# Optimization experiments

Hardware: AMD Instinct MI355X
Metric: run time of the kernel (lower is better)

The kernel has to match this reference:

```python
import jax, jax.numpy as jnp
import numpy as np

N, E, F, H, HEADS, L, G = 16384, 262144, 16, 128, 4, 5, 128
DFF = 4 * H
EPS = 1e-5

def _bn(h, g, b):
    m = h.mean(axis=0)
    v = h.var(axis=0)
    return g * (h - m) / jnp.sqrt(v + EPS) + b

def setup_inputs():
    key = jax.random.key(0)
    ks = jax.random.split(key, 20)
    rn = lambda k, s, fan: jax.random.normal(k, s, jnp.float32) / np.float32(np.sqrt(fan))
    return {
        'x': jax.random.normal(ks[0], (N, F), jnp.float32),
        'edge_index': jax.random.randint(ks[1], (2, E), 0, N),
        'batch_index': jnp.sort(jax.random.randint(ks[2], (N,), 0, G)),
        'embW': rn(ks[3], (F, H), F), 'embb': jnp.zeros((H,), jnp.float32),
        'emb_g': jnp.ones((H,), jnp.float32), 'emb_be': jnp.zeros((H,), jnp.float32),
        'Wq': rn(ks[4], (L, H, HEADS * H), H), 'bq': jnp.zeros((L, HEADS * H), jnp.float32),
        'Wk': rn(ks[5], (L, H, HEADS * H), H), 'bk': jnp.zeros((L, HEADS * H), jnp.float32),
        'Wv': rn(ks[6], (L, H, HEADS * H), H), 'bv': jnp.zeros((L, HEADS * H), jnp.float32),
        'Wskip': rn(ks[7], (L, H, H), H), 'bskip': jnp.zeros((L, H), jnp.float32),
        'Wbeta': rn(ks[8], (L, 3 * H, 1), 3 * H),
        'W1': rn(ks[9], (L, H, DFF), H), 'b1': jnp.zeros((L, DFF), jnp.float32),
        'g1': jnp.ones((L, DFF), jnp.float32), 'be1': jnp.zeros((L, DFF), jnp.float32),
        'W2': rn(ks[10], (L, DFF, H), DFF), 'b2': jnp.zeros((L, H), jnp.float32),
        'predW': rn(ks[11], (H, 1), H), 'predb': jnp.zeros((1,), jnp.float32),
    }

def reference(x, edge_index, batch_index, embW, embb, emb_g, emb_be, Wq, bq, Wk, bk, Wv, bv, Wskip, bskip, Wbeta, W1, b1, g1, be1, W2, b2, predW, predb):
    src, dst = edge_index[0], edge_index[1]
    h = jax.nn.gelu(_bn(x @ embW + embb, emb_g, emb_be), approximate=False)
    scale = jnp.float32(1.0 / np.sqrt(H))  # sqrt(out_channels) per PyG TransformerConv

    def layer(h, p):
        Wq_, bq_, Wk_, bk_, Wv_, bv_, Ws_, bs_, Wb_, W1_, b1_, g1_, be1_, W2_, b2_ = p
        q = (h @ Wq_ + bq_).reshape(N, HEADS, H)
        k = (h @ Wk_ + bk_).reshape(N, HEADS, H)
        v = (h @ Wv_ + bv_).reshape(N, HEADS, H)
        logits = jnp.einsum('ehc,ehc->eh', q[dst], k[src]) * scale  # [E, HEADS]
        m = jax.ops.segment_max(logits, dst, num_segments=N)
        p_e = jnp.exp(logits - m[dst])
        denom = jax.ops.segment_sum(p_e, dst, num_segments=N) + 1e-16
        agg = jax.ops.segment_sum(p_e[:, :, None] * v[src], dst, num_segments=N)
        out = (agg / denom[:, :, None]).mean(axis=1)  # concat=False -> mean over heads
        x_r = h @ Ws_ + bs_
        beta = jax.nn.sigmoid(jnp.concatenate([out, x_r, out - x_r], axis=-1) @ Wb_)  # [N,1]
        out = beta * x_r + (1.0 - beta) * out
        hh = jax.nn.gelu(_bn(out @ W1_ + b1_, g1_, be1_), approximate=False)
        return hh @ W2_ + b2_

    def step(carry, p):
        return layer(carry, p), None

    h, _ = jax.lax.scan(step, h, (Wq, bq, Wk, bk, Wv, bv, Wskip, bskip, Wbeta, W1, b1, g1, be1, W2, b2))
    pooled = jax.ops.segment_max(h, batch_index, num_segments=G)  # MaxAggregation
    return (pooled @ predW + predb).reshape(-1)
```

## Files before the change

### kernel.cpp

```cpp
#include <hip/hip_runtime.h>
#include <hip/hip_bf16.h>

using bf16 = __hip_bfloat16;
typedef __attribute__((ext_vector_type(8))) short bf16x8;
typedef __attribute__((ext_vector_type(4))) float f32x4;

constexpr int N_   = 16384;
constexpr int E_   = 262144;
constexpr int F_   = 16;
constexpr int H_   = 128;
constexpr int NF1_ = 640;
constexpr int DFF_ = 512;
constexpr int G_   = 128;
constexpr int L_   = 5;
constexpr float EPS_ = 1e-5f;

constexpr int WCAT1SZ = NF1_ * 128;
constexpr int W1TSZ   = 512 * 128;
constexpr int W2TSZ   = 512 * 128;
constexpr int WVSSZ   = 128 * 512;
constexpr int TRBLKS  = 5 * 144;

__device__ __forceinline__ float gelu_f(float x) {
  return 0.5f * x * (1.0f + erff(x * 0.70710678118654752440f));
}

__device__ __forceinline__ void unpack8(const uint4 w, float* f) {
  f[0] = __uint_as_float(w.x << 16); f[1] = __uint_as_float(w.x & 0xFFFF0000u);
  f[2] = __uint_as_float(w.y << 16); f[3] = __uint_as_float(w.y & 0xFFFF0000u);
  f[4] = __uint_as_float(w.z << 16); f[5] = __uint_as_float(w.z & 0xFFFF0000u);
  f[6] = __uint_as_float(w.w << 16); f[7] = __uint_as_float(w.w & 0xFFFF0000u);
}

__global__ __launch_bounds__(256) void k_ptrans(
    const float* __restrict__ Ws, const float* __restrict__ W1,
    const float* __restrict__ W2, const float* __restrict__ bs,
    const float* __restrict__ bv,
    bf16* __restrict__ Wcat1, bf16* __restrict__ W1t, bf16* __restrict__ W2t,
    float* __restrict__ bcat, float* __restrict__ bvm) {
  __shared__ float lds[32][33];
  const int b = blockIdx.x;
  if (b >= TRBLKS) {
    int j = (b - TRBLKS) * 256 + threadIdx.x;
    if (j < 5 * NF1_) {
      int l = j / NF1_, c = j % NF1_;
      if (c >= 512) bcat[j] = bs[l * 128 + (c - 512)];
    } else if (j < 5 * NF1_ + 5 * 128) {
      int j2 = j - 5 * NF1_;
      int l = j2 / 128, n = j2 % 128;
      bvm[j2] = 0.25f * (bv[l * 512 + n] + bv[l * 512 + 128 + n]
                       + bv[l * 512 + 256 + n] + bv[l * 512 + 384 + n]);
    }
    return;
  }
  const int l = b / 144, t = b % 144;
  const float* src; int C; bf16* dst; int dld; int nof; int tt;
  if (t < 16) {
    tt = t;
    src = Ws + (size_t)l * 128 * 128; C = 128;
    dst = Wcat1 + (size_t)l * WCAT1SZ; dld = 128; nof = 512;
  } else if (t < 80) {
    tt = t - 16;
    src = W1 + (size_t)l * 128 * 512; C = 512;
    dst = W1t + (size_t)l * W1TSZ; dld = 128; nof = 0;
  } else {
    tt = t - 80;
    src = W2 + (size_t)l * 512 * 128; C = 128;
    dst = W2t + (size_t)l * W2TSZ; dld = 512; nof = 0;
  }
  const int tpr = C >> 5;
  const int r0 = (tt / tpr) * 32, c0 = (tt % tpr) * 32;
  const int j = threadIdx.x & 31, g = threadIdx.x >> 5;
#pragma unroll
  for (int ii = 0; ii < 4; ++ii) {
    int i = g * 4 + ii;
    lds[i][j] = src[(size_t)(r0 + i) * C + c0 + j];
  }
  __syncthreads();
#pragma unroll
  for (int ii = 0; ii < 4; ++ii) {
    int i = g * 4 + ii;
    dst[(size_t)(nof + c0 + i) * dld + r0 + j] = __float2bfloat16(lds[j][i]);
  }
}

__global__ __launch_bounds__(256) void k_wvprep(const float* __restrict__ Wv,
                                                bf16* __restrict__ Wvs) {
  __shared__ float lds[32][33];
  const int b = blockIdx.x;
  const int l = b / 64, rest = b % 64;
  const int h = rest / 16, tt = rest % 16;
  const int r0 = (tt / 4) * 32, c0 = (tt % 4) * 32;
  const float* src = Wv + (size_t)l * 128 * 512 + h * 128;
  bf16* dst = Wvs + (size_t)l * WVSSZ;
  const int j = threadIdx.x & 31, g = threadIdx.x >> 5;
#pragma unroll
  for (int ii = 0; ii < 4; ++ii) {
    int i = g * 4 + ii;
    lds[i][j] = src[(size_t)(r0 + i) * 512 + c0 + j];
  }
  __syncthreads();
#pragma unroll
  for (int ii = 0; ii < 4; ++ii) {
    int i = g * 4 + ii;
    dst[(size_t)(c0 + i) * 512 + h * 128 + r0 + j] = __float2bfloat16(0.25f * lds[j][i]);
  }
}

__global__ __launch_bounds__(256) void k_gmat(
    const float* __restrict__ Wq, const float* __restrict__ Wk,
    const float* __restrict__ bq,
    bf16* __restrict__ Wcat1, float* __restrict__ bcat) {
  __shared__ float lq[32][132];
  __shared__ float lk[32][132];
  const int l = blockIdx.x >> 2, h = blockIdx.x & 3;
  const int half = blockIdx.y;
  const int tid = threadIdx.x;
  const int c = tid & 127, ch = tid >> 7;
  const int cp0 = half * 64 + ch * 32;
  const float* wqL = Wq + (size_t)l * 128 * 512 + h * 128;
  const float* wkL = Wk + (size_t)l * 128 * 512 + h * 128;
  float acc[32];
#pragma unroll
  for (int j = 0; j < 32; ++j) acc[j] = 0.f;
  for (int a0 = 0; a0 < 128; a0 += 32) {
    __syncthreads();
#pragma unroll
    for (int q4 = 0; q4 < 4; ++q4) {
      int f4 = tid * 4 + q4;
      int row = f4 >> 3, af = f4 & 7;
      float4 gq = *reinterpret_cast<const float4*>(wqL + (size_t)row * 512 + a0 + af * 4);
      float4 gk = *reinterpret_cast<const float4*>(wkL + (size_t)row * 512 + a0 + af * 4);
      lq[af * 4 + 0][row] = gq.x; lq[af * 4 + 1][row] = gq.y;
      lq[af * 4 + 2][row] = gq.z; lq[af * 4 + 3][row] = gq.w;
      lk[af * 4 + 0][row] = gk.x; lk[af * 4 + 1][row] = gk.y;
      lk[af * 4 + 2][row] = gk.z; lk[af * 4 + 3][row] = gk.w;
    }
    __syncthreads();
    for (int a = 0; a < 32; ++a) {
      float wq = lq[a][c];
#pragma unroll
      for (int j = 0; j < 32; ++j) acc[j] = fmaf(wq, lk[a][cp0 + j], acc[j]);
    }
  }
  bf16* gt = Wcat1 + (size_t)l * WCAT1SZ;
#pragma unroll
  for (int j = 0; j < 32; ++j)
    gt[(size_t)(h * 128 + cp0 + j) * 128 + c] = __float2bfloat16(acc[j]);
  if (half == 0 && ch == 0) {
    float s = 0.f;
    const float* wkr = wkL + (size_t)c * 512;
    const float* bqh = bq + (size_t)l * 512 + h * 128;
    for (int a = 0; a < 128; ++a) s = fmaf(wkr[a], bqh[a], s);
    bcat[(size_t)l * NF1_ + h * 128 + c] = s;
  }
}

__global__ __launch_bounds__(256) void k_embed2(const float* __restrict__ x,
    const float* __restrict__ W, const float* __restrict__ b,
    float* __restrict__ out, float* __restrict__ ss, float* __restrict__ sq) {
  __shared__ float xs[128][16];
  __shared__ float wsm[16][128];
  __shared__ float sr[2][128], qr[2][128];
  const int blk = blockIdx.x;
  const int t = threadIdx.x;
  for (int i = t; i < 16 * 128; i += 256) wsm[i >> 7][i & 127] = W[i];
  for (int i = t; i < 128 * 16; i += 256) xs[i >> 4][i & 15] = x[(size_t)blk * 2048 + i];
  __syncthreads();
  const int c = t & 127, rg = t >> 7;
  float bc = b[c];
  float s = 0.f, q = 0.f;
  for (int r = rg * 64; r < rg * 64 + 64; ++r) {
    float v = bc;
#pragma unroll
    for (int f = 0; f < 16; ++f) v = fmaf(xs[r][f], wsm[f][c], v);
    out[(size_t)(blk * 128 + r) * 128 + c] = v;
    s += v; q += v * v;
  }
  sr[rg][c] = s; qr[rg][c] = q;
  __syncthreads();
  if (t < 128) { ss[blk * 128 + t] = sr[0][t] + sr[1][t]; sq[blk * 128 + t] = qr[0][t] + qr[1][t]; }
}

template<int NC, int NP>
__global__ void k_bn_finalize(const float* __restrict__ sums, const float* __restrict__ sumsq,
                              const float* __restrict__ g, const float* __restrict__ be,
                              float* __restrict__ a, float* __restrict__ cc) {
  int c = blockIdx.x * 128 + threadIdx.x;
  if (c >= NC) return;
  float s = 0.f, q = 0.f;
  for (int b = 0; b < NP; ++b) { s += sums[(size_t)b * NC + c]; q += sumsq[(size_t)b * NC + c]; }
  float mean = s * (1.0f / N_);
  float var  = q * (1.0f / N_) - mean * mean;
  float inv  = rsqrtf(var + EPS_);
  float aa   = g[c] * inv;
  a[c]  = aa;
  cc[c] = be[c] - aa * mean;
}

template<int NC>
__global__ void k_bn_apply_gelu_cast(const float* __restrict__ xin, const float* __restrict__ a,
                                     const float* __restrict__ cc, bf16* __restrict__ outb) {
  int i4 = (blockIdx.x * 256 + threadIdx.x) * 4;
  int c = i4 & (NC - 1);
  float4 v = *reinterpret_cast<const float4*>(xin + i4);
  union { uint2 u2; bf16 h[4]; } pk;
  pk.h[0] = __float2bfloat16(gelu_f(fmaf(a[c + 0], v.x, cc[c + 0])));
  pk.h[1] = __float2bfloat16(gelu_f(fmaf(a[c + 1], v.y, cc[c + 1])));
  pk.h[2] = __float2bfloat16(gelu_f(fmaf(a[c + 2], v.z, cc[c + 2])));
  pk.h[3] = __float2bfloat16(gelu_f(fmaf(a[c + 3], v.w, cc[c + 3])));
  *reinterpret_cast<uint2*>(outb + i4) = pk.u2;
}

__global__ void k_count(const int* __restrict__ dst, int* __restrict__ deg) {
  int e = blockIdx.x * 256 + threadIdx.x;
  if (e < E_) atomicAdd(&deg[dst[e]], 1);
}

__global__ void k_bsum(const int* __restrict__ deg, int* __restrict__ bsum) {
  __shared__ int sh[256];
  int t = threadIdx.x;
  sh[t] = deg[blockIdx.x * 256 + t];
  __syncthreads();
  for (int d = 128; d > 0; d >>= 1) { if (t < d) sh[t] += sh[t + d]; __syncthreads(); }
  if (t == 0) bsum[blockIdx.x] = sh[0];
}

__global__ void k_boffs(const int* __restrict__ deg, const int* __restrict__ bsum,
                        int* __restrict__ offs) {
  __shared__ int sh[256];
  __shared__ int baseSh;
  int t = threadIdx.x;
  if (t < 64) {
    int v = bsum[t];
    int s = v;
    for (int d = 1; d < 64; d <<= 1) { int o = __shfl_up(s, d); if (t >= d) s += o; }
    if (t == (int)blockIdx.x) baseSh = s - v;
  }
  int v = deg[blockIdx.x * 256 + t];
  sh[t] = v;
  __syncthreads();
  for (int d = 1; d < 256; d <<= 1) {
    int add = (t >= d) ? sh[t - d] : 0;
    __syncthreads();
    sh[t] += add;
    __syncthreads();
  }
  offs[blockIdx.x * 256 + t] = baseSh + sh[t] - v;
  if (blockIdx.x == 63 && t == 255) offs[N_] = E_;
}

__global__ void k_scatter(const int* __restrict__ src, const int* __restrict__ dst,
                          const int* __restrict__ off, int* __restrict__ cursor,
                          int* __restrict__ srcs) {
  int e = blockIdx.x * 256 + threadIdx.x;
  if (e < E_) {
    int d = dst[e];
    int pos = off[d] + atomicAdd(&cursor[d], 1);
    srcs[pos] = src[e];
  }
}

template<int KDIM, int NOUT, int TM, int MODE>
__global__ __launch_bounds__(256) void k_mfma(
    const bf16* __restrict__ A, const bf16* __restrict__ BT,
    const float* __restrict__ bias,
    float* __restrict__ outF,
    float* __restrict__ zfp, float* __restrict__ xrp,
    float* __restrict__ ss, float* __restrict__ sq) {
  constexpr int MF = TM / 32;
  __shared__ bf16 As[TM][72];
  __shared__ bf16 Bs[128][72];
  __shared__ float sred[2][128], qred[2][128];
  const int tid = threadIdx.x;
  const int wid = tid >> 6, lane = tid & 63;
  const int wr = wid >> 1, wc = wid & 1;
  const int m0 = blockIdx.x * TM, n0 = blockIdx.y * 128;
  const int ln = lane & 15, lq = lane >> 4;
  f32x4 acc[MF][4];
#pragma unroll
  for (int i = 0; i < MF; ++i)
#pragma unroll
    for (int j = 0; j < 4; ++j) acc[i][j] = (f32x4){0.f, 0.f, 0.f, 0.f};

  for (int k0 = 0; k0 < KDIM; k0 += 64) {
#pragma unroll
    for (int u = tid; u < TM * 8; u += 256) {
      int r = u >> 3, c = u & 7;
      *(uint4*)(&As[r][c * 8]) = *(const uint4*)(A + (size_t)(m0 + r) * KDIM + k0 + c * 8);
    }
#pragma unroll
    for (int u = tid; u < 1024; u += 256) {
      int r = u >> 3, c = u & 7;
      *(uint4*)(&Bs[r][c * 8]) = *(const uint4*)(BT + (size_t)(n0 + r) * KDIM + k0 + c * 8);
    }
    __syncthreads();
#pragma unroll
    for (int kk = 0; kk < 2; ++kk) {
      bf16x8 af[MF], bg[4];
#pragma unroll
      for (int i = 0; i < MF; ++i)
        af[i] = *(const bf16x8*)(&As[wr * (TM / 2) + i * 16 + ln][kk * 32 + lq * 8]);
#pragma unroll
      for (int j = 0; j < 4; ++j)
        bg[j] = *(const bf16x8*)(&Bs[wc * 64 + j * 16 + ln][kk * 32 + lq * 8]);
#pragma unroll
      for (int i = 0; i < MF; ++i)
#pragma unroll
        for (int j = 0; j < 4; ++j)
          acc[i][j] = __builtin_amdgcn_mfma_f32_16x16x32_bf16(af[i], bg[j], acc[i][j], 0, 0, 0);
    }
    __syncthreads();
  }
  float ssj[4] = {0.f, 0.f, 0.f, 0.f}, sqj[4] = {0.f, 0.f, 0.f, 0.f};
#pragma unroll
  for (int i = 0; i < MF; ++i) {
#pragma unroll
    for (int j = 0; j < 4; ++j) {
      int gcol = n0 + wc * 64 + j * 16 + ln;
      float bv = bias[gcol];
      int row0 = m0 + wr * (TM / 2) + i * 16 + lq * 4;
#pragma unroll
      for (int qq = 0; qq < 4; ++qq) {
        float val = acc[i][j][qq] + bv;
        int row = row0 + qq;
        if (MODE == 3) {
          outF[(size_t)row * NOUT + gcol] = val;
          ssj[j] += val; sqj[j] += val * val;
        } else {
          if (gcol < 512) zfp[(size_t)row * 512 + gcol] = val;
          else            xrp[(size_t)row * H_ + (gcol - 512)] = val;
        }
      }
    }
  }
  if constexpr (MODE == 3) {
#pragma unroll
    for (int j = 0; j < 4; ++j) {
      ssj[j] += __shfl_xor(ssj[j], 16); ssj[j] += __shfl_xor(ssj[j], 32);
      sqj[j] += __shfl_xor(sqj[j], 16); sqj[j] += __shfl_xor(sqj[j], 32);
    }
    if (lq == 0) {
#pragma unroll
      for (int j = 0; j < 4; ++j) {
        sred[wr][wc * 64 + j * 16 + ln] = ssj[j];
        qred[wr][wc * 64 + j * 16 + ln] = sqj[j];
      }
    }
    __syncthreads();
    if (tid < 128) {
      ss[(size_t)blockIdx.x * NOUT + n0 + tid] = sred[0][tid] + sred[1][tid];
      sq[(size_t)blockIdx.x * NOUT + n0 + tid] = qred[0][tid] + qred[1][tid];
    }
  }
}

template<int KDIM, int NOUT, int CSPL, int MODE>
__global__ __launch_bounds__(256) void k_sgemm(
    const bf16* __restrict__ A, const bf16* __restrict__ BT,
    const float* __restrict__ bias,
    float* __restrict__ outF, bf16* __restrict__ outB) {
  constexpr int KS = KDIM / 32;
  constexpr int NCOL = NOUT / CSPL;
  constexpr int NFR = NCOL / 16;
  __shared__ bf16 Bs[NFR][KS][64][8];
  const int tid = threadIdx.x;
  const int wid = tid >> 6, lane = tid & 63;
  const int ln = lane & 15, lq = lane >> 4;
  const int nc0 = blockIdx.y * NCOL;
  for (int idx = tid; idx < NCOL * (KDIM / 8); idx += 256) {
    int col = idx / (KDIM / 8);
    int oct = idx % (KDIM / 8);
    uint4 w = *(const uint4*)(BT + (size_t)(nc0 + col) * KDIM + oct * 8);
    int ks = oct >> 2, q = oct & 3;
    *(uint4*)(&Bs[col >> 4][ks][q * 16 + (col & 15)][0]) = w;
  }
  __syncthreads();
  const int m0 = blockIdx.x * 64 + wid * 16;
  bf16x8 a[KS];
  const bf16* ap = A + (size_t)(m0 + ln) * KDIM + lq * 8;
#pragma unroll
  for (int ks = 0; ks < KS; ++ks) a[ks] = *(const bf16x8*)(ap + ks * 32);
  const int orow = m0 + lq * 4;
#pragma unroll
  for (int nf = 0; nf < NFR; ++nf) {
    f32x4 acc0 = (f32x4){0.f, 0.f, 0.f, 0.f};
    f32x4 acc1 = (f32x4){0.f, 0.f, 0.f, 0.f};
#pragma unroll
    for (int ks = 0; ks < KS; ks += 2) {
      acc0 = __builtin_amdgcn_mfma_f32_16x16x32_bf16(a[ks],     *(const bf16x8*)(&Bs[nf][ks][lane][0]),     acc0, 0, 0, 0);
      acc1 = __builtin_amdgcn_mfma_f32_16x16x32_bf16(a[ks + 1], *(const bf16x8*)(&Bs[nf][ks + 1][lane][0]), acc1, 0, 0, 0);
    }
    const int col = nc0 + nf * 16 + ln;
    float bv = 0.f;
    if constexpr (MODE == 6) bv = bias[col];
    float v0 = (acc0[0] + acc1[0]) + bv;
    float v1 = (acc0[1] + acc1[1]) + bv;
    float v2 = (acc0[2] + acc1[2]) + bv;
    float v3 = (acc0[3] + acc1[3]) + bv;
    outF[(size_t)(orow + 0) * NOUT + col] = v0;
    outF[(size_t)(orow + 1) * NOUT + col] = v1;
    outF[(size_t)(orow + 2) * NOUT + col] = v2;
    outF[(size_t)(orow + 3) * NOUT + col] = v3;
    if constexpr (MODE == 6) {
      outB[(size_t)(orow + 0) * NOUT + col] = __float2bfloat16(v0);
      outB[(size_t)(orow + 1) * NOUT + col] = __float2bfloat16(v1);
      outB[(size_t)(orow + 2) * NOUT + col] = __float2bfloat16(v2);
      outB[(size_t)(orow + 3) * NOUT + col] = __float2bfloat16(v3);
    }
  }
}

__global__ __launch_bounds__(256) void k_attn(const float* __restrict__ zf,
    const bf16* __restrict__ hb, const int* __restrict__ srcs,
    const int* __restrict__ off, bf16* __restrict__ aggB) {
  const int wave = threadIdx.x >> 6;
  const int lane = threadIdx.x & 63;
  const int bid = blockIdx.x;
  const int swz = ((bid & 7) << 9) | (bid >> 3);
  const int node = swz * 4 + wave;
  const int sub = lane & 15;
  const float scale = 0.08838834764831845f;
  float qf[8];
  {
    const float4* qp = reinterpret_cast<const float4*>(zf + (size_t)node * 512) + lane * 2;
    float4 a = qp[0], b = qp[1];
    qf[0]=a.x; qf[1]=a.y; qf[2]=a.z; qf[3]=a.w;
    qf[4]=b.x; qf[5]=b.y; qf[6]=b.z; qf[7]=b.w;
  }
  float m = -1e30f, den = 0.f;
  float acc[8] = {0.f, 0.f, 0.f, 0.f, 0.f, 0.f, 0.f, 0.f};
  const int s0 = off[node], s1 = off[node + 1];
  if (s0 < s1) {
    int i0 = srcs[s0];
    int i1 = (s0 + 1 < s1) ? srcs[s0 + 1] : i0;
    uint4 h0 = *(const uint4*)(hb + (size_t)i0 * 128 + sub * 8);
    uint4 h1 = *(const uint4*)(hb + (size_t)i1 * 128 + sub * 8);
    for (int t = s0; t < s1; t += 2) {
      int j0 = (t + 2 < s1) ? srcs[t + 2] : i0;
      int j1 = (t + 3 < s1) ? srcs[t + 3] : i0;
      uint4 nh0 = *(const uint4*)(hb + (size_t)j0 * 128 + sub * 8);
      uint4 nh1 = *(const uint4*)(hb + (size_t)j1 * 128 + sub * 8);
      {
        float hf[8]; unpack8(h0, hf);
        float p = hf[0]*qf[0]+hf[1]*qf[1]+hf[2]*qf[2]+hf[3]*qf[3]
                + hf[4]*qf[4]+hf[5]*qf[5]+hf[6]*qf[6]+hf[7]*qf[7];
        p += __shfl_xor(p, 1); p += __shfl_xor(p, 2);
        p += __shfl_xor(p, 4); p += __shfl_xor(p, 8);
        float logit = p * scale;
        if (logit > m + 8.f) {
          float co = __expf(m - logit);
          den *= co;
#pragma unroll
          for (int j = 0; j < 8; ++j) acc[j] *= co;
          m = logit;
        }
        float pe = __expf(logit - m);
        den += pe;
#pragma unroll
        for (int j = 0; j < 8; ++j) acc[j] = fmaf(pe, hf[j], acc[j]);
      }
      if (t + 1 < s1) {
        float hf[8]; unpack8(h1, hf);
        float p = hf[0]*qf[0]+hf[1]*qf[1]+hf[2]*qf[2]+hf[3]*qf[3]
                + hf[4]*qf[4]+hf[5]*qf[5]+hf[6]*qf[6]+hf[7]*qf[7];
        p += __shfl_xor(p, 1); p += __shfl_xor(p, 2);
        p += __shfl_xor(p, 4); p += __shfl_xor(p, 8);
        float logit = p * scale;
        if (logit > m + 8.f) {
          float co = __expf(m - logit);
          den *= co;
#pragma unroll
          for (int j = 0; j < 8; ++j) acc[j] *= co;
          m = logit;
        }
        float pe = __expf(logit - m);
        den += pe;
#pragma unroll
        for (int j = 0; j < 8; ++j) acc[j] = fmaf(pe, hf[j], acc[j]);
      }
      h0 = nh0; h1 = nh1;
    }
  }
  float inv = 1.f / (den + 1e-16f);
  union { uint4 u4; bf16 h[8]; } pk;
#pragma unroll
  for (int j = 0; j < 8; ++j) pk.h[j] = __float2bfloat16(acc[j] * inv);
  *reinterpret_cast<uint4*>(aggB + (size_t)node * 512 + lane * 8) = pk.u4;
}

__global__ __launch_bounds__(256) void k_beta(const float* __restrict__ out0,
    const float* __restrict__ xr, const float* __restrict__ Wb,
    const float* __restrict__ bvm, const int* __restrict__ off,
    bf16* __restrict__ gated) {
  const int wave = threadIdx.x >> 6;
  const int lane = threadIdx.x & 63;
  const int node = blockIdx.x * 4 + wave;
  const int c0 = lane * 2;
  bool hasE = off[node + 1] > off[node];
  const size_t base = (size_t)node * H_ + c0;
  float2 o = *reinterpret_cast<const float2*>(out0 + base);
  if (hasE) { o.x += bvm[c0]; o.y += bvm[c0 + 1]; }
  float2 xv = *reinterpret_cast<const float2*>(xr + base);
  float s = o.x * (Wb[c0] + Wb[256 + c0]) + xv.x * (Wb[128 + c0] - Wb[256 + c0])
          + o.y * (Wb[c0 + 1] + Wb[256 + c0 + 1]) + xv.y * (Wb[128 + c0 + 1] - Wb[256 + c0 + 1]);
#pragma unroll
  for (int d = 1; d < 64; d <<= 1) s += __shfl_xor(s, d);
  float beta = 1.f / (1.f + __expf(-s));
  union { unsigned u; bf16 h[2]; } pk;
  pk.h[0] = __float2bfloat16(beta * xv.x + (1.f - beta) * o.x);
  pk.h[1] = __float2bfloat16(beta * xv.y + (1.f - beta) * o.y);
  *reinterpret_cast<unsigned*>(gated + base) = pk.u;
}

__global__ __launch_bounds__(256) void k_poolpred(const float* __restrict__ h,
    const int* __restrict__ batch, const float* __restrict__ predW,
    const float* __restrict__ predb, float* __restrict__ out) {
  __shared__ float cm[2][128];
  __shared__ int range[2];
  const int g = blockIdx.x, t = threadIdx.x;
  if (t < 2) {
    int target = g + t;
    int lo = 0, hi = N_;
    while (lo < hi) { int mid = (lo + hi) >> 1; if (batch[mid] < target) lo = mid + 1; else hi = mid; }
    range[t] = lo;
  }
  __syncthreads();
  const int lo = range[0], hi = range[1];
  const int c = t & 127, rg = t >> 7;
  float m = -3.402823466e+38f;
  for (int r = lo + rg; r < hi; r += 2) m = fmaxf(m, h[(size_t)r * H_ + c]);
  cm[rg][c] = m;
  __syncthreads();
  if (t < 64) {
    float m0 = fmaxf(cm[0][t], cm[1][t]);
    float m1 = fmaxf(cm[0][t + 64], cm[1][t + 64]);
    float s = m0 * predW[t] + m1 * predW[t + 64];
#pragma unroll
    for (int d = 1; d < 64; d <<= 1) s += __shfl_xor(s, d);
    if (t == 0) out[g] = s + predb[0];
  }
}

extern "C" void kernel_launch(void* const* d_in, const int* in_sizes, int n_in,
                              void* d_out, int out_size, void* d_ws, size_t ws_size,
                              hipStream_t stream) {
  const float* x      = (const float*)d_in[0];
  const int*   edge   = (const int*)d_in[1];
  const int*   esrc   = edge;
  const int*   edst   = edge + E_;
  const int*   batch  = (const int*)d_in[2];
  const float* embW   = (const float*)d_in[3];
  const float* embb   = (const float*)d_in[4];
  const float* emb_g  = (const float*)d_in[5];
  const float* emb_be = (const float*)d_in[6];
  const float* Wq     = (const float*)d_in[7];
  const float* bq     = (const float*)d_in[8];
  const float* Wk     = (const float*)d_in[9];
  const float* Wv     = (const float*)d_in[11];
  const float* bv     = (const float*)d_in[12];
  const float* Wskip  = (const float*)d_in[13];
  const float* bskip  = (const float*)d_in[14];
  const float* Wbeta  = (const float*)d_in[15];
  const float* W1     = (const float*)d_in[16];
  const float* b1     = (const float*)d_in[17];
  const float* g1     = (const float*)d_in[18];
  const float* be1    = (const float*)d_in[19];
  const float* W2     = (const float*)d_in[20];
  const float* b2     = (const float*)d_in[21];
  const float* predW  = (const float*)d_in[22];
  const float* predb  = (const float*)d_in[23];

  float* ws = (float*)d_ws;
  size_t o = 0;
  auto alloc_f = [&](size_t n) { float* p = ws + o; o += n; return p; };
  float* A32   = alloc_f((size_t)N_ * 512);
  float* B32   = alloc_f((size_t)N_ * H_);
  float* xr    = alloc_f((size_t)N_ * H_);
  float* stats = alloc_f((size_t)2 * 128 * DFF_);
  float* a_c   = alloc_f(DFF_);
  float* c_c   = alloc_f(DFF_);
  float* bcat  = alloc_f(5 * NF1_);
  float* bvm   = alloc_f(5 * 128);
  bf16* bp = (bf16*)(ws + o);
  size_t ob = 0;
  auto alloc_b = [&](size_t n) { bf16* p = bp + ob; ob += n; return p; };
  bf16* aggB = alloc_b((size_t)N_ * 512);
  bf16* hb   = alloc_b((size_t)N_ * H_);
  bf16* gated= alloc_b((size_t)N_ * H_);
  bf16* Wcat1= alloc_b((size_t)5 * WCAT1SZ);
  bf16* W1t  = alloc_b((size_t)5 * W1TSZ);
  bf16* W2t  = alloc_b((size_t)5 * W2TSZ);
  bf16* Wvs  = alloc_b((size_t)5 * WVSSZ);
  int* deg    = (int*)(bp + ob);
  int* offs   = deg + N_;
  int* cursor = offs + N_ + 1;
  int* srcs   = cursor + N_;
  int* bsum   = srcs + E_;

  float* zf   = A32;  float* t1 = A32;
  float* out0 = B32;  float* h32 = B32;
  bf16*  t1b  = aggB;

  k_ptrans<<<TRBLKS + 15, 256, 0, stream>>>(Wskip, W1, W2, bskip, bv,
                                            Wcat1, W1t, W2t, bcat, bvm);
  k_wvprep<<<320, 256, 0, stream>>>(Wv, Wvs);
  k_gmat<<<dim3(20, 2), 256, 0, stream>>>(Wq, Wk, bq, Wcat1, bcat);

  hipMemsetAsync(deg, 0, N_ * sizeof(int), stream);
  hipMemsetAsync(cursor, 0, N_ * sizeof(int), stream);
  k_count  <<<E_ / 256, 256, 0, stream>>>(edst, deg);
  k_bsum   <<<64, 256, 0, stream>>>(deg, bsum);
  k_boffs  <<<64, 256, 0, stream>>>(deg, bsum, offs);
  k_scatter<<<E_ / 256, 256, 0, stream>>>(esrc, edst, offs, cursor, srcs);

  k_embed2<<<128, 256, 0, stream>>>(x, embW, embb, A32, stats, stats + 128 * 128);
  k_bn_finalize<128, 128><<<1, 128, 0, stream>>>(stats, stats + 128 * 128, emb_g, emb_be, a_c, c_c);
  k_bn_apply_gelu_cast<128><<<N_ * H_ / 1024, 256, 0, stream>>>(A32, a_c, c_c, hb);

  for (int l = 0; l < L_; ++l) {
    const float* Wb_ = Wbeta + (size_t)l * 3 * H_;
    const float* b1_ = b1 + (size_t)l * DFF_;
    const float* g1_ = g1 + (size_t)l * DFF_;
    const float* be1_= be1 + (size_t)l * DFF_;
    const float* b2_ = b2 + (size_t)l * H_;

    k_mfma<128, NF1_, 128, 2><<<dim3(N_ / 128, NF1_ / 128), 256, 0, stream>>>(
        hb, Wcat1 + (size_t)l * WCAT1SZ, bcat + (size_t)l * NF1_,
        nullptr, zf, xr, nullptr, nullptr);

    k_attn<<<N_ / 4, 256, 0, stream>>>(zf, hb, srcs, offs, aggB);

    k_sgemm<512, 128, 2, 5><<<dim3(N_ / 64, 2), 256, 0, stream>>>(
        aggB, Wvs + (size_t)l * WVSSZ, nullptr, out0, nullptr);

    k_beta<<<N_ / 4, 256, 0, stream>>>(out0, xr, Wb_, bvm + (size_t)l * 128, offs, gated);

    k_mfma<128, 512, 128, 3><<<dim3(N_ / 128, 4), 256, 0, stream>>>(
        gated, W1t + (size_t)l * W1TSZ, b1_,
        t1, nullptr, nullptr, stats, stats + 128 * 512);

    k_bn_finalize<512, 128><<<4, 128, 0, stream>>>(
        stats, stats + 128 * 512, g1_, be1_, a_c, c_c);

    k_bn_apply_gelu_cast<512><<<N_ * DFF_ / 1024, 256, 0, stream>>>(t1, a_c, c_c, t1b);

    k_sgemm<512, 128, 2, 6><<<dim3(N_ / 64, 2), 256, 0, stream>>>(
        t1b, W2t + (size_t)l * W2TSZ, b2_, h32, hb);
  }

  k_poolpred<<<G_, 256, 0, stream>>>(h32, batch, predW, predb, (float*)d_out);
}
```

Measured before the change: 685.5 us.

## Fuse BN-apply+GELU into W2 GEMM and move QKV GEMM to register-A sgemm

The separate BN-apply/GELU/bf16-cast pass over the 16384x512 FFN hidden tensor is removed. The W2 GEMM now reads fp32 t1 directly and applies the per-column affine, erf GELU and bf16 cast while loading its A fragments. The first per-layer projection GEMM (hb x Wcat1 into zf/xr) moves from the tiled LDS k_mfma kernel to the k_sgemm kernel, which keeps A in registers with a 5-way column split. The fused W2 path reads fp32 instead of bf16 and computes GELU redundantly in each of the two column-split blocks, trading one kernel and its round trip for extra reads and erf work.

```diff
diff --git a/kernel.cpp b/kernel.cpp
--- a/kernel.cpp
+++ b/kernel.cpp
@@ -266,7 +266,6 @@
     const bf16* __restrict__ A, const bf16* __restrict__ BT,
     const float* __restrict__ bias,
     float* __restrict__ outF,
-    float* __restrict__ zfp, float* __restrict__ xrp,
     float* __restrict__ ss, float* __restrict__ sq) {
   constexpr int MF = TM / 32;
   __shared__ bf16 As[TM][72];
@@ -324,46 +323,42 @@
       for (int qq = 0; qq < 4; ++qq) {
         float val = acc[i][j][qq] + bv;
         int row = row0 + qq;
-        if (MODE == 3) {
-          outF[(size_t)row * NOUT + gcol] = val;
-          ssj[j] += val; sqj[j] += val * val;
-        } else {
-          if (gcol < 512) zfp[(size_t)row * 512 + gcol] = val;
-          else            xrp[(size_t)row * H_ + (gcol - 512)] = val;
-        }
+        outF[(size_t)row * NOUT + gcol] = val;
+        ssj[j] += val; sqj[j] += val * val;
       }
     }
   }
-  if constexpr (MODE == 3) {
+#pragma unroll
+  for (int j = 0; j < 4; ++j) {
+    ssj[j] += __shfl_xor(ssj[j], 16); ssj[j] += __shfl_xor(ssj[j], 32);
+    sqj[j] += __shfl_xor(sqj[j], 16); sqj[j] += __shfl_xor(sqj[j], 32);
+  }
+  if (lq == 0) {
 #pragma unroll
     for (int j = 0; j < 4; ++j) {
-      ssj[j] += __shfl_xor(ssj[j], 16); ssj[j] += __shfl_xor(ssj[j], 32);
-      sqj[j] += __shfl_xor(sqj[j], 16); sqj[j] += __shfl_xor(sqj[j], 32);
-    }
-    if (lq == 0) {
-#pragma unroll
-      for (int j = 0; j < 4; ++j) {
-        sred[wr][wc * 64 + j * 16 + ln] = ssj[j];
-        qred[wr][wc * 64 + j * 16 + ln] = sqj[j];
-      }
-    }
-    __syncthreads();
-    if (tid < 128) {
-      ss[(size_t)blockIdx.x * NOUT + n0 + tid] = sred[0][tid] + sred[1][tid];
-      sq[(size_t)blockIdx.x * NOUT + n0 + tid] = qred[0][tid] + qred[1][tid];
-    }
+      sred[wr][wc * 64 + j * 16 + ln] = ssj[j];
+      qred[wr][wc * 64 + j * 16 + ln] = sqj[j];
+    }
+  }
+  __syncthreads();
+  if (tid < 128) {
+    ss[(size_t)blockIdx.x * NOUT + n0 + tid] = sred[0][tid] + sred[1][tid];
+    sq[(size_t)blockIdx.x * NOUT + n0 + tid] = qred[0][tid] + qred[1][tid];
   }
 }
 
 template<int KDIM, int NOUT, int CSPL, int MODE>
 __global__ __launch_bounds__(256) void k_sgemm(
-    const bf16* __restrict__ A, const bf16* __restrict__ BT,
-    const float* __restrict__ bias,
-    float* __restrict__ outF, bf16* __restrict__ outB) {
+    const bf16* __restrict__ A, const float* __restrict__ Af,
+    const bf16* __restrict__ BT, const float* __restrict__ bias,
+    float* __restrict__ outF, bf16* __restrict__ outB,
+    float* __restrict__ zfp, float* __restrict__ xrp,
+    const float* __restrict__ aCol, const float* __restrict__ cCol) {
   constexpr int KS = KDIM / 32;
   constexpr int NCOL = NOUT / CSPL;
   constexpr int NFR = NCOL / 16;
   __shared__ bf16 Bs[NFR][KS][64][8];
+  __shared__ float aS[MODE == 7 ? KDIM : 1], cS[MODE == 7 ? KDIM : 1];
   const int tid = threadIdx.x;
   const int wid = tid >> 6, lane = tid & 63;
   const int ln = lane & 15, lq = lane >> 4;
@@ -375,12 +370,31 @@
     int ks = oct >> 2, q = oct & 3;
     *(uint4*)(&Bs[col >> 4][ks][q * 16 + (col & 15)][0]) = w;
   }
+  if constexpr (MODE == 7) {
+    for (int i = tid; i < KDIM; i += 256) { aS[i] = aCol[i]; cS[i] = cCol[i]; }
+  }
   __syncthreads();
   const int m0 = blockIdx.x * 64 + wid * 16;
   bf16x8 a[KS];
-  const bf16* ap = A + (size_t)(m0 + ln) * KDIM + lq * 8;
-#pragma unroll
-  for (int ks = 0; ks < KS; ++ks) a[ks] = *(const bf16x8*)(ap + ks * 32);
+  if constexpr (MODE == 7) {
+    const float* ap = Af + (size_t)(m0 + ln) * KDIM + lq * 8;
+#pragma unroll
+    for (int ks = 0; ks < KS; ++ks) {
+      float4 f0 = *(const float4*)(ap + ks * 32);
+      float4 f1 = *(const float4*)(ap + ks * 32 + 4);
+      float f[8] = {f0.x, f0.y, f0.z, f0.w, f1.x, f1.y, f1.z, f1.w};
+      int colb = lq * 8 + ks * 32;
+      union { bf16x8 v; bf16 h[8]; } pk;
+#pragma unroll
+      for (int j = 0; j < 8; ++j)
+        pk.h[j] = __float2bfloat16(gelu_f(fmaf(aS[colb + j], f[j], cS[colb + j])));
+      a[ks] = pk.v;
+    }
+  } else {
+    const bf16* ap = A + (size_t)(m0 + ln) * KDIM + lq * 8;
+#pragma unroll
+    for (int ks = 0; ks < KS; ++ks) a[ks] = *(const bf16x8*)(ap + ks * 32);
+  }
   const int orow = m0 + lq * 4;
 #pragma unroll
   for (int nf = 0; nf < NFR; ++nf) {
@@ -393,20 +407,35 @@
     }
     const int col = nc0 + nf * 16 + ln;
     float bv = 0.f;
-    if constexpr (MODE == 6) bv = bias[col];
+    if constexpr (MODE != 5) bv = bias[col];
     float v0 = (acc0[0] + acc1[0]) + bv;
     float v1 = (acc0[1] + acc1[1]) + bv;
     float v2 = (acc0[2] + acc1[2]) + bv;
     float v3 = (acc0[3] + acc1[3]) + bv;
-    outF[(size_t)(orow + 0) * NOUT + col] = v0;
-    outF[(size_t)(orow + 1) * NOUT + col] = v1;
-    outF[(size_t)(orow + 2) * NOUT + col] = v2;
-    outF[(size_t)(orow + 3) * NOUT + col] = v3;
-    if constexpr (MODE == 6) {
-      outB[(size_t)(orow + 0) * NOUT + col] = __float2bfloat16(v0);
-      outB[(size_t)(orow + 1) * NOUT + col] = __float2bfloat16(v1);
-      outB[(size_t)(orow + 2) * NOUT + col] = __float2bfloat16(v2);
-      outB[(size_t)(orow + 3) * NOUT + col] = __float2bfloat16(v3);
+    if constexpr (MODE == 2) {
+      if (col < 512) {
+        zfp[(size_t)(orow + 0) * 512 + col] = v0;
+        zfp[(size_t)(orow + 1) * 512 + col] = v1;
+        zfp[(size_t)(orow + 2) * 512 + col] = v2;
+        zfp[(size_t)(orow + 3) * 512 + col] = v3;
+      } else {
+        int cx = col - 512;
+        xrp[(size_t)(orow + 0) * 128 + cx] = v0;
+        xrp[(size_t)(orow + 1) * 128 + cx] = v1;
+        xrp[(size_t)(orow + 2) * 128 + cx] = v2;
+        xrp[(size_t)(orow + 3) * 128 + cx] = v3;
+      }
+    } else {
+      outF[(size_t)(orow + 0) * NOUT + col] = v0;
+      outF[(size_t)(orow + 1) * NOUT + col] = v1;
+      outF[(size_t)(orow + 2) * NOUT + col] = v2;
+      outF[(size_t)(orow + 3) * NOUT + col] = v3;
+      if constexpr (MODE == 7) {
+        outB[(size_t)(orow + 0) * NOUT + col] = __float2bfloat16(v0);
+        outB[(size_t)(orow + 1) * NOUT + col] = __float2bfloat16(v1);
+        outB[(size_t)(orow + 2) * NOUT + col] = __float2bfloat16(v2);
+        outB[(size_t)(orow + 3) * NOUT + col] = __float2bfloat16(v3);
+      }
     }
   }
 }
@@ -600,7 +629,6 @@
 
   float* zf   = A32;  float* t1 = A32;
   float* out0 = B32;  float* h32 = B32;
-  bf16*  t1b  = aggB;
 
   k_ptrans<<<TRBLKS + 15, 256, 0, stream>>>(Wskip, W1, W2, bskip, bv,
                                             Wcat1, W1t, W2t, bcat, bvm);
@@ -625,28 +653,27 @@
     const float* be1_= be1 + (size_t)l * DFF_;
     const float* b2_ = b2 + (size_t)l * H_;
 
-    k_mfma<128, NF1_, 128, 2><<<dim3(N_ / 128, NF1_ / 128), 256, 0, stream>>>(
-        hb, Wcat1 + (size_t)l * WCAT1SZ, bcat + (size_t)l * NF1_,
-        nullptr, zf, xr, nullptr, nullptr);
+    k_sgemm<128, NF1_, 5, 2><<<dim3(N_ / 64, 5), 256, 0, stream>>>(
+        hb, nullptr, Wcat1 + (size_t)l * WCAT1SZ, bcat + (size_t)l * NF1_,
+        nullptr, nullptr, zf, xr, nullptr, nullptr);
 
     k_attn<<<N_ / 4, 256, 0, stream>>>(zf, hb, srcs, offs, aggB);
 
     k_sgemm<512, 128, 2, 5><<<dim3(N_ / 64, 2), 256, 0, stream>>>(
-        aggB, Wvs + (size_t)l * WVSSZ, nullptr, out0, nullptr);
+        aggB, nullptr, Wvs + (size_t)l * WVSSZ, nullptr,
+        out0, nullptr, nullptr, nullptr, nullptr, nullptr);
 
     k_beta<<<N_ / 4, 256, 0, stream>>>(out0, xr, Wb_, bvm + (size_t)l * 128, offs, gated);
 
     k_mfma<128, 512, 128, 3><<<dim3(N_ / 128, 4), 256, 0, stream>>>(
-        gated, W1t + (size_t)l * W1TSZ, b1_,
-        t1, nullptr, nullptr, stats, stats + 128 * 512);
+        gated, W1t + (size_t)l * W1TSZ, b1_, t1, stats, stats + 128 * 512);
 
     k_bn_finalize<512, 128><<<4, 128, 0, stream>>>(
         stats, stats + 128 * 512, g1_, be1_, a_c, c_c);
 
-    k_bn_apply_gelu_cast<512><<<N_ * DFF_ / 1024, 256, 0, stream>>>(t1, a_c, c_c, t1b);
-
-    k_sgemm<512, 128, 2, 6><<<dim3(N_ / 64, 2), 256, 0, stream>>>(
-        t1b, W2t + (size_t)l * W2TSZ, b2_, h32, hb);
+    k_sgemm<512, 128, 2, 7><<<dim3(N_ / 64, 2), 256, 0, stream>>>(
+        nullptr, t1, W2t + (size_t)l * W2TSZ, b2_,
+        h32, hb, nullptr, nullptr, a_c, c_c);
   }
 
   k_poolpred<<<G_, 256, 0, stream>>>(h32, batch, predW, predb, (float*)d_out);
```

After: 1.015 ms. 48.1% more time.
